# Kernel tuning notes

Hardware: AMD Instinct MI355X
Metric: run time of the kernel (lower is better)

Reference implementation:

```python
import jax, jax.numpy as jnp
import numpy as np

H, W, C, CLS, R, B = 32, 32, 512, 1000, 64, 128

def setup_inputs() -> dict:
    key = jax.random.key(0)
    k = jax.random.split(key, 6)
    return {
        "x":   jax.random.normal(k[0], (B, C, W, H), dtype=jnp.float32),
        "U1":  jax.random.normal(k[1], (H, R),  dtype=jnp.float32) * 0.1,
        "U2":  jax.random.normal(k[2], (W, R),  dtype=jnp.float32) * 0.1,
        "U3":  jax.random.normal(k[3], (C, R),  dtype=jnp.float32) * 0.1,
        "U4":  jax.random.normal(k[4], (CLS, R), dtype=jnp.float32) * 0.1,
        "lam": jax.random.normal(k[5], (R,),    dtype=jnp.float32) * 0.1,
    }

def reference(x, U1, U2, U3, U4, lam):
    # Original: T[cls,c,w,h] = sum_r lam[r] U4[cls,r] U3[c,r] U2[w,r] U1[h,r]
    # then out[b,cls] = sum_{c,w,h} x[b,c,w,h] * T[cls,c,w,h].
    # Equivalent fused contraction (never materializes the dense CP tensor):
    t = jnp.einsum('bcwh,hr->bcwr', x, U1)      # contract h
    t = jnp.einsum('bcwr,wr->bcr', t, U2)       # contract w
    t = jnp.einsum('bcr,cr->br', t, U3)         # contract c
    out = jnp.einsum('br,r,Cr->bC', t, lam, U4) # scale by lam, expand classes
    return out
```

## Files before the change

### kernel.cpp

```cpp
#include <hip/hip_runtime.h>
#include <stdint.h>

#define HH 32
#define WW 32
#define CC 512
#define CLS 1000
#define RR 64
#define BB 128
#define KK 1024
#define MM (BB*CC)

#define KSPLIT 4
#define KS (KK/KSPLIT)
#define QS (KS/32)

typedef __bf16  bf16x8 __attribute__((ext_vector_type(8)));
typedef float   f32x4  __attribute__((ext_vector_type(4)));
typedef uint32_t u32x4 __attribute__((ext_vector_type(4)));

__global__ void prep_v(const float* __restrict__ U1, const float* __restrict__ U2,
                       __bf16* __restrict__ Vf) {
    int idx = blockIdx.x * 256 + threadIdx.x;
    int l  = idx & 63;
    int qf = idx >> 6;
    int f  = qf & 3;
    int q  = qf >> 2;
    int n  = f * 16 + (l & 15);
    int kb = q * 32 + (l >> 4) * 8;
#pragma unroll
    for (int j = 0; j < 8; ++j) {
        int k = kb + j;
        int w = k >> 5, h = k & 31;
        float v = U2[w * RR + n] * U1[h * RR + n];
        Vf[(size_t)idx * 8 + j] = (__bf16)v;
    }
}

__global__ void __launch_bounds__(256)
main_k(const float* __restrict__ x, const __bf16* __restrict__ Vf,
       const float* __restrict__ U3, float* __restrict__ t3) {
    __shared__ alignas(16) __bf16 vs[QS * 4 * 64 * 8];
    __shared__ float red[4][64];

    {
        const u32x4* src = (const u32x4*)(Vf + (size_t)blockIdx.y * QS * 4 * 64 * 8);
        u32x4* dst = (u32x4*)vs;
#pragma unroll
        for (int i = 0; i < 8; ++i)
            dst[threadIdx.x + i * 256] = src[threadIdx.x + i * 256];
    }
    __syncthreads();

    const int tid = threadIdx.x;
    const int wv  = tid >> 6;
    const int l   = tid & 63;
    const int m   = blockIdx.x * 64 + wv * 16 + (l & 15);
    const int k0  = blockIdx.y * KS;

    const float* xp = x + (size_t)m * KK + k0 + ((l >> 4) * 8);

    f32x4 acc[4] = {};

#pragma unroll
    for (int q = 0; q < QS; ++q) {
        f32x4 a0 = *(const f32x4*)(xp + q * 32);
        f32x4 a1 = *(const f32x4*)(xp + q * 32 + 4);
        bf16x8 af;
        af[0] = (__bf16)a0.x; af[1] = (__bf16)a0.y;
        af[2] = (__bf16)a0.z; af[3] = (__bf16)a0.w;
        af[4] = (__bf16)a1.x; af[5] = (__bf16)a1.y;
        af[6] = (__bf16)a1.z; af[7] = (__bf16)a1.w;
#pragma unroll
        for (int f = 0; f < 4; ++f) {
            bf16x8 bf = ((const bf16x8*)vs)[(q * 4 + f) * 64 + l];
            acc[f] = __builtin_amdgcn_mfma_f32_16x16x32_bf16(af, bf, acc[f], 0, 0, 0);
        }
    }

    const int b      = blockIdx.x >> 3;
    const int c_base = (blockIdx.x * 64) & (CC - 1);
    const int c_l    = c_base + wv * 16 + (l >> 4) * 4;

    float p[4];
#pragma unroll
    for (int f = 0; f < 4; ++f) {
        int r = f * 16 + (l & 15);
        float s = 0.f;
#pragma unroll
        for (int i = 0; i < 4; ++i)
            s += acc[f][i] * U3[(c_l + i) * RR + r];
        p[f] = s;
    }
#pragma unroll
    for (int f = 0; f < 4; ++f) {
        p[f] += __shfl_xor(p[f], 16, 64);
        p[f] += __shfl_xor(p[f], 32, 64);
    }
    if (l < 16) {
#pragma unroll
        for (int f = 0; f < 4; ++f) red[wv][f * 16 + l] = p[f];
    }
    __syncthreads();
    if (tid < 64) {
        float s = red[0][tid] + red[1][tid] + red[2][tid] + red[3][tid];
        atomicAdd(&t3[b * RR + tid], s);
    }
}

__global__ void out_k(const float* __restrict__ t3, const float* __restrict__ lam,
                      const float* __restrict__ U4, float* __restrict__ out) {
    __shared__ float sl[RR];
    const int b = blockIdx.y;
    const int tid = threadIdx.x;
    if (tid < RR) sl[tid] = t3[b * RR + tid] * lam[tid];
    __syncthreads();
    const int cls = blockIdx.x * 256 + tid;
    if (cls < CLS) {
        const f32x4* u4 = (const f32x4*)(U4 + (size_t)cls * RR);
        float s = 0.f;
#pragma unroll
        for (int i = 0; i < 16; ++i) {
            f32x4 v = u4[i];
            s += v.x * sl[i*4+0] + v.y * sl[i*4+1] + v.z * sl[i*4+2] + v.w * sl[i*4+3];
        }
        out[b * CLS + cls] = s;
    }
}

extern "C" void kernel_launch(void* const* d_in, const int* in_sizes, int n_in,
                              void* d_out, int out_size, void* d_ws, size_t ws_size,
                              hipStream_t stream) {
    const float* x   = (const float*)d_in[0];
    const float* U1  = (const float*)d_in[1];
    const float* U2  = (const float*)d_in[2];
    const float* U3  = (const float*)d_in[3];
    const float* U4  = (const float*)d_in[4];
    const float* lam = (const float*)d_in[5];

    __bf16* Vf = (__bf16*)d_ws;
    float*  t3 = (float*)((char*)d_ws + 128 * 1024);
    float*  out = (float*)d_out;

    hipMemsetAsync(t3, 0, BB * RR * sizeof(float), stream);
    prep_v<<<32, 256, 0, stream>>>(U1, U2, Vf);
    main_k<<<dim3(MM / 64, KSPLIT), 256, 0, stream>>>(x, Vf, U3, t3);
    out_k<<<dim3(4, BB), 256, 0, stream>>>(t3, lam, U4, out);
}
```

Before: 388.6 us.

## Replace atomic accumulation with partial buffers reduced in output kernel

The main kernel now writes per-block partial sums for each (part, batch) into a workspace buffer instead of using atomicAdd. This removes the memset and the atomic contention. The output kernel sums the 32 partials and processes 16 batches per block, which lets each thread reuse its U4 row held in registers. The U3 loads are hoisted before the MFMA loop so they overlap with the shared-memory fill. In exchange the workspace grows, the output kernel launches fewer blocks, and register pressure rises in both kernels.

```diff
diff --git a/kernel.cpp b/kernel.cpp
--- a/kernel.cpp
+++ b/kernel.cpp
@@ -13,6 +13,7 @@
 #define KSPLIT 4
 #define KS (KK/KSPLIT)
 #define QS (KS/32)
+#define NPART 32
 
 typedef __bf16  bf16x8 __attribute__((ext_vector_type(8)));
 typedef float   f32x4  __attribute__((ext_vector_type(4)));
@@ -38,7 +39,7 @@
 
 __global__ void __launch_bounds__(256)
 main_k(const float* __restrict__ x, const __bf16* __restrict__ Vf,
-       const float* __restrict__ U3, float* __restrict__ t3) {
+       const float* __restrict__ U3, float* __restrict__ t3p) {
     __shared__ alignas(16) __bf16 vs[QS * 4 * 64 * 8];
     __shared__ float red[4][64];
 
@@ -49,7 +50,6 @@
         for (int i = 0; i < 8; ++i)
             dst[threadIdx.x + i * 256] = src[threadIdx.x + i * 256];
     }
-    __syncthreads();
 
     const int tid = threadIdx.x;
     const int wv  = tid >> 6;
@@ -59,8 +59,19 @@
 
     const float* xp = x + (size_t)m * KK + k0 + ((l >> 4) * 8);
 
+    const int c_l = ((blockIdx.x * 64) & (CC - 1)) + wv * 16 + (l >> 4) * 4;
+    float u3r[4][4];
+#pragma unroll
+    for (int f = 0; f < 4; ++f) {
+        int r = f * 16 + (l & 15);
+#pragma unroll
+        for (int i = 0; i < 4; ++i)
+            u3r[f][i] = U3[(c_l + i) * RR + r];
+    }
+
+    __syncthreads();
+
     f32x4 acc[4] = {};
-
 #pragma unroll
     for (int q = 0; q < QS; ++q) {
         f32x4 a0 = *(const f32x4*)(xp + q * 32);
@@ -77,18 +88,13 @@
         }
     }
 
-    const int b      = blockIdx.x >> 3;
-    const int c_base = (blockIdx.x * 64) & (CC - 1);
-    const int c_l    = c_base + wv * 16 + (l >> 4) * 4;
-
     float p[4];
 #pragma unroll
     for (int f = 0; f < 4; ++f) {
-        int r = f * 16 + (l & 15);
         float s = 0.f;
 #pragma unroll
         for (int i = 0; i < 4; ++i)
-            s += acc[f][i] * U3[(c_l + i) * RR + r];
+            s += acc[f][i] * u3r[f][i];
         p[f] = s;
     }
 #pragma unroll
@@ -102,28 +108,49 @@
     }
     __syncthreads();
     if (tid < 64) {
+        const int b    = blockIdx.x >> 3;
+        const int part = blockIdx.y * 8 + (blockIdx.x & 7);
         float s = red[0][tid] + red[1][tid] + red[2][tid] + red[3][tid];
-        atomicAdd(&t3[b * RR + tid], s);
+        t3p[((size_t)part * BB + b) * RR + tid] = s;
     }
 }
 
-__global__ void out_k(const float* __restrict__ t3, const float* __restrict__ lam,
+__global__ void out_k(const float* __restrict__ t3p, const float* __restrict__ lam,
                       const float* __restrict__ U4, float* __restrict__ out) {
-    __shared__ float sl[RR];
-    const int b = blockIdx.y;
+    __shared__ float sl[16 * RR];
     const int tid = threadIdx.x;
-    if (tid < RR) sl[tid] = t3[b * RR + tid] * lam[tid];
+    const int by  = blockIdx.y;
+
+    {
+        const int bl = tid >> 4;
+        const int rg = tid & 15;
+        const int b  = by * 16 + bl;
+        f32x4 s = {};
+#pragma unroll
+        for (int p = 0; p < NPART; ++p)
+            s += *(const f32x4*)(t3p + ((size_t)p * BB + b) * RR + rg * 4);
+        const f32x4 lm = *(const f32x4*)(lam + rg * 4);
+        s *= lm;
+        *(f32x4*)(sl + bl * RR + rg * 4) = s;
+    }
     __syncthreads();
+
     const int cls = blockIdx.x * 256 + tid;
-    if (cls < CLS) {
-        const f32x4* u4 = (const f32x4*)(U4 + (size_t)cls * RR);
+    if (cls >= CLS) return;
+    f32x4 u[16];
+    const f32x4* u4 = (const f32x4*)(U4 + (size_t)cls * RR);
+#pragma unroll
+    for (int i = 0; i < 16; ++i) u[i] = u4[i];
+#pragma unroll
+    for (int bl = 0; bl < 16; ++bl) {
+        const float* s0 = sl + bl * RR;
         float s = 0.f;
 #pragma unroll
         for (int i = 0; i < 16; ++i) {
-            f32x4 v = u4[i];
-            s += v.x * sl[i*4+0] + v.y * sl[i*4+1] + v.z * sl[i*4+2] + v.w * sl[i*4+3];
+            f32x4 v = u[i];
+            s += v.x * s0[i*4+0] + v.y * s0[i*4+1] + v.z * s0[i*4+2] + v.w * s0[i*4+3];
         }
-        out[b * CLS + cls] = s;
+        out[(size_t)(by * 16 + bl) * CLS + cls] = s;
     }
 }
 
@@ -137,12 +164,11 @@
     const float* U4  = (const float*)d_in[4];
     const float* lam = (const float*)d_in[5];
 
-    __bf16* Vf = (__bf16*)d_ws;
-    float*  t3 = (float*)((char*)d_ws + 128 * 1024);
+    __bf16* Vf  = (__bf16*)d_ws;
+    float*  t3p = (float*)((char*)d_ws + 128 * 1024);
     float*  out = (float*)d_out;
 
-    hipMemsetAsync(t3, 0, BB * RR * sizeof(float), stream);
     prep_v<<<32, 256, 0, stream>>>(U1, U2, Vf);
-    main_k<<<dim3(MM / 64, KSPLIT), 256, 0, stream>>>(x, Vf, U3, t3);
-    out_k<<<dim3(4, BB), 256, 0, stream>>>(t3, lam, U4, out);
+    main_k<<<dim3(MM / 64, KSPLIT), 256, 0, stream>>>(x, Vf, U3, t3p);
+    out_k<<<dim3(4, 8), 256, 0, stream>>>(t3p, lam, U4, out);
 }
```

Result: slower. 399.3 us (+2.8%).
